# Kernel tuning notes

Measured on AMD Instinct MI355X. Metric: run time of the kernel, lower is better.

## Reference

```python
import jax, jax.numpy as jnp
import numpy as np

NUM_HEADS = 8
EPS = 1e-5


def setup_inputs() -> dict:
    key = jax.random.key(0)
    ks = jax.random.split(key, 12)
    B, S, D = 16384, 12, 512
    s = 1.0 / np.sqrt(D)
    return {
        "x": jax.random.normal(ks[0], (B, S, D), dtype=jnp.float32),
        "Wq": jax.random.uniform(ks[1], (D, D), jnp.float32, -s, s),
        "bq": jax.random.uniform(ks[2], (D,), jnp.float32, -s, s),
        "Wk": jax.random.uniform(ks[3], (D, D), jnp.float32, -s, s),
        "bk": jax.random.uniform(ks[4], (D,), jnp.float32, -s, s),
        "Wv": jax.random.uniform(ks[5], (D, D), jnp.float32, -s, s),
        "bv": jax.random.uniform(ks[6], (D,), jnp.float32, -s, s),
        "adj_bias": jnp.zeros((NUM_HEADS, S, S), dtype=jnp.float32),
        "Wo": jax.random.uniform(ks[7], (D, D), jnp.float32, -s, s),
        "bo": jax.random.uniform(ks[8], (D,), jnp.float32, -s, s),
        "gamma": jnp.ones((D,), dtype=jnp.float32),
        "beta": jnp.zeros((D,), dtype=jnp.float32),
    }


def reference(x, Wq, bq, Wk, bk, Wv, bv, adj_bias, Wo, bo, gamma, beta):
    B, S, D = x.shape
    H = NUM_HEADS
    hd = D // H
    # QKV projections -> (B, H, S, hd)
    def proj(W, b):
        return (jnp.einsum('bsd,de->bse', x, W) + b).reshape(B, S, H, hd).transpose(0, 2, 1, 3)
    q = proj(Wq, bq)
    k = proj(Wk, bk)
    v = proj(Wv, bv)
    # scores with learned adjacency bias: (B, H, S, S)
    scores = jnp.einsum('bhsd,bhtd->bhst', q, k) / np.sqrt(hd).astype(np.float32)
    scores = scores + adj_bias[None, :, :S, :S]
    attn = jax.nn.softmax(scores, axis=-1)  # dropout is identity in eval mode
    out = jnp.einsum('bhst,bhtd->bhsd', attn, v)
    out = out.transpose(0, 2, 1, 3).reshape(B, S, D)
    out = jnp.einsum('bsd,de->bse', out, Wo) + bo
    # residual (in_dim == out_dim) + LayerNorm
    y = out + x
    mu = jnp.mean(y, axis=-1, keepdims=True)
    var = jnp.mean(jnp.square(y - mu), axis=-1, keepdims=True)
    return (y - mu) * jax.lax.rsqrt(var + EPS) * gamma + beta
```

## Files before the change

kernel.cpp:

```cpp
#include <hip/hip_runtime.h>
#include <hip/hip_bf16.h>

#define D_DIM 512
#define S_LEN 12
#define H_NUM 8
#define WMAT 262144

#define G_B1 8
#define ROWS1 96
#define THREADS1 768
#define X_OFF   0
#define Q_OFF   98304
#define K_OFF   110592
#define V_OFF   122880
#define P_OFF   135168
#define SMEM1   142848

#define G_B2 4
#define ROWS2 48
#define THREADS2 512
#define AST_OFF 0
#define RED_OFF 49152
#define MU_OFF  52416
#define SMEM2   52800

typedef __attribute__((ext_vector_type(8))) short bf16x8;
typedef __attribute__((ext_vector_type(4))) float f32x4;

__device__ __forceinline__ unsigned short f2bf(float f) {
    union { float f; unsigned u; } c; c.f = f;
    unsigned r = c.u + 0x7fffu + ((c.u >> 16) & 1u);
    return (unsigned short)(r >> 16);
}
__device__ __forceinline__ float bf2f(unsigned short u) {
    union { unsigned u; float f; } c; c.u = ((unsigned)u) << 16;
    return c.f;
}
__device__ __forceinline__ int xswc(int row, int col) {
    return row * 512 + (((col >> 3) ^ (row & 7)) << 3) + (col & 7);
}
__device__ __forceinline__ int qsw(int row, int col) {
    return row * 64 + (((col >> 3) ^ (row & 7)) << 3) + (col & 7);
}

__global__ void prep_weights(const float* __restrict__ Wq, const float* __restrict__ Wk,
                             const float* __restrict__ Wv, const float* __restrict__ Wo,
                             unsigned short* __restrict__ wt) {
    int idx = blockIdx.x * 256 + threadIdx.x;
    int mat = idx >> 18;
    int rem = idx & (WMAT - 1);
    int e = rem >> 9, d = rem & 511;
    const float* W = (mat == 0) ? Wq : (mat == 1) ? Wk : (mat == 2) ? Wv : Wo;
    wt[idx] = f2bf(W[d * D_DIM + e]);
}

__global__ __launch_bounds__(THREADS1, 3) void qkv_attn(
    const float* __restrict__ x, const unsigned short* __restrict__ wt,
    const float* __restrict__ bq, const float* __restrict__ bk, const float* __restrict__ bv,
    const float* __restrict__ adj, float* __restrict__ aout)
{
    extern __shared__ char smem[];
    unsigned short* Xh = (unsigned short*)(smem + X_OFF);
    unsigned short* Qh = (unsigned short*)(smem + Q_OFF);
    unsigned short* Kh = (unsigned short*)(smem + K_OFF);
    unsigned short* Vh = (unsigned short*)(smem + V_OFF);
    float* Pl = (float*)(smem + P_OFF);

    const int tid  = threadIdx.x;
    const int lane = tid & 63;
    const int w    = tid >> 6;
    const int lr   = lane & 15;
    const int lg   = lane >> 4;
    const int lr12 = (lr < 12) ? lr : 11;
    const size_t row0 = (size_t)blockIdx.x * ROWS1;

    #pragma unroll
    for (int it = 0; it < 16; ++it) {
        int idx = it * THREADS1 + tid;
        int r = idx >> 7, col = (idx & 127) << 2;
        float4 v = *(const float4*)(x + (row0 + r) * (size_t)D_DIM + col);
        ushort4 pk;
        pk.x = f2bf(v.x); pk.y = f2bf(v.y); pk.z = f2bf(v.z); pk.w = f2bf(v.w);
        *(ushort4*)(Xh + xswc(r, col)) = pk;
    }
    __syncthreads();

    const int mat  = w >> 2;
    const int colt = w & 3;
    const int colh = colt * 16 + lr;
    const float* bsel = (mat == 0) ? bq : (mat == 1) ? bk : bv;
    unsigned short* T = (mat == 0) ? Qh : (mat == 1) ? Kh : Vh;
    const int rb = w * S_LEN;

    #pragma unroll 1
    for (int h = 0; h < H_NUM; ++h) {
        f32x4 acc[6];
        #pragma unroll
        for (int mt = 0; mt < 6; ++mt) acc[mt] = (f32x4){0.f, 0.f, 0.f, 0.f};

        const unsigned short* bAp = wt + (size_t)mat * WMAT + (h * 64 + colh) * D_DIM + lg * 8;
        bf16x8 bc = *(const bf16x8*)(bAp);
        #pragma unroll
        for (int ks = 0; ks < 16; ++ks) {
            bf16x8 bn;
            if (ks < 15) bn = *(const bf16x8*)(bAp + (ks + 1) * 32);
            #pragma unroll
            for (int mt = 0; mt < 6; ++mt) {
                bf16x8 af = *(const bf16x8*)(Xh + xswc(mt * 16 + lr, ks * 32 + lg * 8));
                acc[mt] = __builtin_amdgcn_mfma_f32_16x16x32_bf16(af, bc, acc[mt], 0, 0, 0);
            }
            if (ks < 15) bc = bn;
        }
        {
            float bias = bsel[h * 64 + colh];
            #pragma unroll
            for (int mt = 0; mt < 6; ++mt)
                #pragma unroll
                for (int j = 0; j < 4; ++j)
                    T[qsw(mt * 16 + lg * 4 + j, colh)] = f2bf(acc[mt][j] + bias);
        }
        __syncthreads();

        if (w < 8) {
            f32x4 sacc = (f32x4){0.f, 0.f, 0.f, 0.f};
            #pragma unroll
            for (int k2 = 0; k2 < 2; ++k2) {
                bf16x8 ak = *(const bf16x8*)(Kh + qsw(rb + lr12, k2 * 32 + lg * 8));
                bf16x8 aq = *(const bf16x8*)(Qh + qsw(rb + lr12, k2 * 32 + lg * 8));
                sacc = __builtin_amdgcn_mfma_f32_16x16x32_bf16(ak, aq, sacc, 0, 0, 0);
            }
            float ab4[4] = {0.f, 0.f, 0.f, 0.f};
            if (lg < 3 && lr < 12) {
                float4 t4 = *(const float4*)(adj + (h * S_LEN + lr) * S_LEN + lg * 4);
                ab4[0] = t4.x; ab4[1] = t4.y; ab4[2] = t4.z; ab4[3] = t4.w;
            }
            float sc[4], e4[4];
            float m = -1e30f;
            #pragma unroll
            for (int j = 0; j < 4; ++j) {
                int t = lg * 4 + j;
                sc[j] = (t < 12) ? (sacc[j] * 0.125f + ab4[j]) : -1e30f;
                m = fmaxf(m, sc[j]);
            }
            m = fmaxf(m, __shfl_xor(m, 16));
            m = fmaxf(m, __shfl_xor(m, 32));
            float ssum = 0.f;
            #pragma unroll
            for (int j = 0; j < 4; ++j) { e4[j] = __expf(sc[j] - m); ssum += e4[j]; }
            ssum += __shfl_xor(ssum, 16);
            ssum += __shfl_xor(ssum, 32);
            float inv = 1.f / ssum;
            float* Pw = Pl + w * 240;
            if (lr < 12 && lg < 3) {
                f32x4 pvec = (f32x4){e4[0] * inv, e4[1] * inv, e4[2] * inv, e4[3] * inv};
                *(f32x4*)(Pw + lr * 20 + lg * 4) = pvec;
            }
            float vv[12];
            #pragma unroll
            for (int t = 0; t < 12; ++t) vv[t] = bf2f(Vh[qsw(rb + t, lane)]);
            #pragma unroll
            for (int ss = 0; ss < 12; ++ss) {
                f32x4 pa = *(const f32x4*)(Pw + ss * 20);
                f32x4 pb = *(const f32x4*)(Pw + ss * 20 + 4);
                f32x4 pc = *(const f32x4*)(Pw + ss * 20 + 8);
                float o = 0.f;
                #pragma unroll
                for (int t = 0; t < 4; ++t) o += pa[t] * vv[t];
                #pragma unroll
                for (int t = 0; t < 4; ++t) o += pb[t] * vv[4 + t];
                #pragma unroll
                for (int t = 0; t < 4; ++t) o += pc[t] * vv[8 + t];
                aout[(row0 + rb + ss) * (size_t)D_DIM + h * 64 + lane] = o;
            }
        }
        __syncthreads();
    }
}

__global__ __launch_bounds__(THREADS2, 2) void oproj_ln(
    const float* __restrict__ x, const unsigned short* __restrict__ wt,
    const float* __restrict__ bo, const float* __restrict__ gamma,
    const float* __restrict__ beta, float* __restrict__ out)
{
    extern __shared__ char smem[];
    unsigned short* Ast = (unsigned short*)(smem + AST_OFF);
    float* red   = (float*)(smem + RED_OFF);
    float* musig = (float*)(smem + MU_OFF);

    const int tid  = threadIdx.x;
    const int lane = tid & 63;
    const int w    = tid >> 6;
    const int lr   = lane & 15;
    const int lg   = lane >> 4;
    const size_t row0 = (size_t)blockIdx.x * ROWS2;

    #pragma unroll
    for (int it = 0; it < 12; ++it) {
        int idx = it * THREADS2 + tid;
        int r = idx >> 7, col = (idx & 127) << 2;
        float4 v = *(const float4*)(out + (row0 + r) * (size_t)D_DIM + col);
        ushort4 pk;
        pk.x = f2bf(v.x); pk.y = f2bf(v.y); pk.z = f2bf(v.z); pk.w = f2bf(v.w);
        *(ushort4*)(Ast + xswc(r, col)) = pk;
    }
    __syncthreads();

    f32x4 Y[3][4];
    #pragma unroll
    for (int mt = 0; mt < 3; ++mt)
        #pragma unroll
        for (int nt = 0; nt < 4; ++nt) Y[mt][nt] = (f32x4){0.f, 0.f, 0.f, 0.f};

    const unsigned short* obase = wt + (size_t)3 * WMAT + (w * 64 + lr) * D_DIM;
    #pragma unroll 2
    for (int ks = 0; ks < 16; ++ks) {
        bf16x8 afr[3];
        #pragma unroll
        for (int mt = 0; mt < 3; ++mt)
            afr[mt] = *(const bf16x8*)(Ast + xswc(mt * 16 + lr, ks * 32 + lg * 8));
        #pragma unroll
        for (int nt = 0; nt < 4; ++nt) {
            bf16x8 bfr = *(const bf16x8*)(obase + nt * 16 * D_DIM + ks * 32 + lg * 8);
            #pragma unroll
            for (int mt = 0; mt < 3; ++mt)
                Y[mt][nt] = __builtin_amdgcn_mfma_f32_16x16x32_bf16(afr[mt], bfr, Y[mt][nt], 0, 0, 0);
        }
    }

    float bo4[4], gm4[4], bt4[4];
    int cols[4];
    #pragma unroll
    for (int nt = 0; nt < 4; ++nt) {
        cols[nt] = w * 64 + nt * 16 + lr;
        bo4[nt] = bo[cols[nt]]; gm4[nt] = gamma[cols[nt]]; bt4[nt] = beta[cols[nt]];
    }
    #pragma unroll
    for (int mt = 0; mt < 3; ++mt)
        #pragma unroll
        for (int j = 0; j < 4; ++j) {
            int rowl = mt * 16 + lg * 4 + j;
            const float* xrow = x + (row0 + rowl) * (size_t)D_DIM;
            float ps = 0.f, pq = 0.f;
            #pragma unroll
            for (int nt = 0; nt < 4; ++nt) {
                float y = Y[mt][nt][j] + bo4[nt] + xrow[cols[nt]];
                Y[mt][nt][j] = y;
                ps += y; pq += y * y;
            }
            ps += __shfl_xor(ps, 1); pq += __shfl_xor(pq, 1);
            ps += __shfl_xor(ps, 2); pq += __shfl_xor(pq, 2);
            ps += __shfl_xor(ps, 4); pq += __shfl_xor(pq, 4);
            ps += __shfl_xor(ps, 8); pq += __shfl_xor(pq, 8);
            if (lr == 0) { red[rowl * 17 + w * 2] = ps; red[rowl * 17 + w * 2 + 1] = pq; }
        }
    __syncthreads();
    if (tid < ROWS2) {
        float s = 0.f, q = 0.f;
        #pragma unroll
        for (int w8 = 0; w8 < 8; ++w8) { s += red[tid * 17 + w8 * 2]; q += red[tid * 17 + w8 * 2 + 1]; }
        float mu = s * (1.f / 512.f);
        float var = q * (1.f / 512.f) - mu * mu;
        musig[tid * 2] = mu;
        musig[tid * 2 + 1] = rsqrtf(var + 1e-5f);
    }
    __syncthreads();
    #pragma unroll
    for (int mt = 0; mt < 3; ++mt)
        #pragma unroll
        for (int j = 0; j < 4; ++j) {
            int rowl = mt * 16 + lg * 4 + j;
            float mu = musig[rowl * 2], rs = musig[rowl * 2 + 1];
            float* orow = out + (row0 + rowl) * (size_t)D_DIM;
            #pragma unroll
            for (int nt = 0; nt < 4; ++nt)
                orow[cols[nt]] = (Y[mt][nt][j] - mu) * rs * gm4[nt] + bt4[nt];
        }
}

extern "C" void kernel_launch(void* const* d_in, const int* in_sizes, int n_in,
                              void* d_out, int out_size, void* d_ws, size_t ws_size,
                              hipStream_t stream) {
    (void)in_sizes; (void)n_in; (void)out_size; (void)ws_size;
    const float* x     = (const float*)d_in[0];
    const float* Wq    = (const float*)d_in[1];
    const float* bq    = (const float*)d_in[2];
    const float* Wk    = (const float*)d_in[3];
    const float* bk    = (const float*)d_in[4];
    const float* Wv    = (const float*)d_in[5];
    const float* bv    = (const float*)d_in[6];
    const float* adj   = (const float*)d_in[7];
    const float* Wo    = (const float*)d_in[8];
    const float* bo    = (const float*)d_in[9];
    const float* gamma = (const float*)d_in[10];
    const float* beta  = (const float*)d_in[11];
    unsigned short* wt = (unsigned short*)d_ws;
    float* outf = (float*)d_out;

    prep_weights<<<4096, 256, 0, stream>>>(Wq, Wk, Wv, Wo, wt);
    qkv_attn<<<16384 / G_B1, THREADS1, SMEM1, stream>>>(x, wt, bq, bk, bv, adj, outf);
    oproj_ln<<<16384 / G_B2, THREADS2, SMEM2, stream>>>(x, wt, bo, gamma, beta, outf);
}
```

Baseline: 1.095 ms.

## Pad Q/K smem rows, store V transposed, widen oproj block to 96 rows

In the attention kernel, Q and K rows in shared memory are padded to a stride of 72, and V is stored transposed with a stride of 102. This is meant to cut LDS bank conflicts on the score MFMA loads and on the per-lane V reads in the PV loop. The output-projection/LayerNorm kernel now uses 1024-thread blocks over 96 rows, with each wave covering 32 columns and 6 row tiles. That halves weight fragment loads per row, at the cost of more shared memory (about 111 KB) and lower occupancy.

```diff
diff --git a/kernel.cpp b/kernel.cpp
--- a/kernel.cpp
+++ b/kernel.cpp
@@ -9,20 +9,22 @@
 #define G_B1 8
 #define ROWS1 96
 #define THREADS1 768
+#define QS 72
+#define VS 102
 #define X_OFF   0
 #define Q_OFF   98304
-#define K_OFF   110592
-#define V_OFF   122880
-#define P_OFF   135168
-#define SMEM1   142848
-
-#define G_B2 4
-#define ROWS2 48
-#define THREADS2 512
+#define K_OFF   112128
+#define V_OFF   125952
+#define P_OFF   139008
+#define SMEM1   146688
+
+#define G_B2 8
+#define ROWS2 96
+#define THREADS2 1024
 #define AST_OFF 0
-#define RED_OFF 49152
-#define MU_OFF  52416
-#define SMEM2   52800
+#define RED_OFF 98304
+#define MU_OFF  110976
+#define SMEM2   111744
 
 typedef __attribute__((ext_vector_type(8))) short bf16x8;
 typedef __attribute__((ext_vector_type(4))) float f32x4;
@@ -39,8 +41,8 @@
 __device__ __forceinline__ int xswc(int row, int col) {
     return row * 512 + (((col >> 3) ^ (row & 7)) << 3) + (col & 7);
 }
-__device__ __forceinline__ int qsw(int row, int col) {
-    return row * 64 + (((col >> 3) ^ (row & 7)) << 3) + (col & 7);
+__device__ __forceinline__ int qsw72(int row, int col) {
+    return row * QS + (((col >> 3) ^ (row & 7)) << 3) + (col & 7);
 }
 
 __global__ void prep_weights(const float* __restrict__ Wq, const float* __restrict__ Wk,
@@ -63,7 +65,7 @@
     unsigned short* Xh = (unsigned short*)(smem + X_OFF);
     unsigned short* Qh = (unsigned short*)(smem + Q_OFF);
     unsigned short* Kh = (unsigned short*)(smem + K_OFF);
-    unsigned short* Vh = (unsigned short*)(smem + V_OFF);
+    unsigned short* Vt = (unsigned short*)(smem + V_OFF);
     float* Pl = (float*)(smem + P_OFF);
 
     const int tid  = threadIdx.x;
@@ -89,7 +91,6 @@
     const int colt = w & 3;
     const int colh = colt * 16 + lr;
     const float* bsel = (mat == 0) ? bq : (mat == 1) ? bk : bv;
-    unsigned short* T = (mat == 0) ? Qh : (mat == 1) ? Kh : Vh;
     const int rb = w * S_LEN;
 
     #pragma unroll 1
@@ -113,11 +114,24 @@
         }
         {
             float bias = bsel[h * 64 + colh];
-            #pragma unroll
-            for (int mt = 0; mt < 6; ++mt)
-                #pragma unroll
-                for (int j = 0; j < 4; ++j)
-                    T[qsw(mt * 16 + lg * 4 + j, colh)] = f2bf(acc[mt][j] + bias);
+            if (mat == 2) {
+                #pragma unroll
+                for (int mt = 0; mt < 6; ++mt) {
+                    int rbase = mt * 16 + lg * 4;
+                    ushort2 p0, p1;
+                    p0.x = f2bf(acc[mt][0] + bias); p0.y = f2bf(acc[mt][1] + bias);
+                    p1.x = f2bf(acc[mt][2] + bias); p1.y = f2bf(acc[mt][3] + bias);
+                    *(ushort2*)(Vt + colh * VS + rbase)     = p0;
+                    *(ushort2*)(Vt + colh * VS + rbase + 2) = p1;
+                }
+            } else {
+                unsigned short* T = (mat == 0) ? Qh : Kh;
+                #pragma unroll
+                for (int mt = 0; mt < 6; ++mt)
+                    #pragma unroll
+                    for (int j = 0; j < 4; ++j)
+                        T[qsw72(mt * 16 + lg * 4 + j, colh)] = f2bf(acc[mt][j] + bias);
+            }
         }
         __syncthreads();
 
@@ -125,8 +139,8 @@
             f32x4 sacc = (f32x4){0.f, 0.f, 0.f, 0.f};
             #pragma unroll
             for (int k2 = 0; k2 < 2; ++k2) {
-                bf16x8 ak = *(const bf16x8*)(Kh + qsw(rb + lr12, k2 * 32 + lg * 8));
-                bf16x8 aq = *(const bf16x8*)(Qh + qsw(rb + lr12, k2 * 32 + lg * 8));
+                bf16x8 ak = *(const bf16x8*)(Kh + qsw72(rb + lr12, k2 * 32 + lg * 8));
+                bf16x8 aq = *(const bf16x8*)(Qh + qsw72(rb + lr12, k2 * 32 + lg * 8));
                 sacc = __builtin_amdgcn_mfma_f32_16x16x32_bf16(ak, aq, sacc, 0, 0, 0);
             }
             float ab4[4] = {0.f, 0.f, 0.f, 0.f};
@@ -157,7 +171,7 @@
             }
             float vv[12];
             #pragma unroll
-            for (int t = 0; t < 12; ++t) vv[t] = bf2f(Vh[qsw(rb + t, lane)]);
+            for (int t = 0; t < 12; ++t) vv[t] = bf2f(Vt[lane * VS + rb + t]);
             #pragma unroll
             for (int ss = 0; ss < 12; ++ss) {
                 f32x4 pa = *(const f32x4*)(Pw + ss * 20);
@@ -177,7 +191,7 @@
     }
 }
 
-__global__ __launch_bounds__(THREADS2, 2) void oproj_ln(
+__global__ __launch_bounds__(THREADS2) void oproj_ln(
     const float* __restrict__ x, const unsigned short* __restrict__ wt,
     const float* __restrict__ bo, const float* __restrict__ gamma,
     const float* __restrict__ beta, float* __restrict__ out)
@@ -205,45 +219,45 @@
     }
     __syncthreads();
 
-    f32x4 Y[3][4];
-    #pragma unroll
-    for (int mt = 0; mt < 3; ++mt)
-        #pragma unroll
-        for (int nt = 0; nt < 4; ++nt) Y[mt][nt] = (f32x4){0.f, 0.f, 0.f, 0.f};
-
-    const unsigned short* obase = wt + (size_t)3 * WMAT + (w * 64 + lr) * D_DIM;
+    f32x4 Y[6][2];
+    #pragma unroll
+    for (int mt = 0; mt < 6; ++mt)
+        #pragma unroll
+        for (int nt = 0; nt < 2; ++nt) Y[mt][nt] = (f32x4){0.f, 0.f, 0.f, 0.f};
+
+    const unsigned short* obase = wt + (size_t)3 * WMAT + (w * 32 + lr) * D_DIM;
     #pragma unroll 2
     for (int ks = 0; ks < 16; ++ks) {
-        bf16x8 afr[3];
-        #pragma unroll
-        for (int mt = 0; mt < 3; ++mt)
+        bf16x8 afr[6];
+        #pragma unroll
+        for (int mt = 0; mt < 6; ++mt)
             afr[mt] = *(const bf16x8*)(Ast + xswc(mt * 16 + lr, ks * 32 + lg * 8));
         #pragma unroll
-        for (int nt = 0; nt < 4; ++nt) {
+        for (int nt = 0; nt < 2; ++nt) {
             bf16x8 bfr = *(const bf16x8*)(obase + nt * 16 * D_DIM + ks * 32 + lg * 8);
             #pragma unroll
-            for (int mt = 0; mt < 3; ++mt)
+            for (int mt = 0; mt < 6; ++mt)
                 Y[mt][nt] = __builtin_amdgcn_mfma_f32_16x16x32_bf16(afr[mt], bfr, Y[mt][nt], 0, 0, 0);
         }
     }
 
-    float bo4[4], gm4[4], bt4[4];
-    int cols[4];
-    #pragma unroll
-    for (int nt = 0; nt < 4; ++nt) {
-        cols[nt] = w * 64 + nt * 16 + lr;
-        bo4[nt] = bo[cols[nt]]; gm4[nt] = gamma[cols[nt]]; bt4[nt] = beta[cols[nt]];
-    }
-    #pragma unroll
-    for (int mt = 0; mt < 3; ++mt)
+    float bo2[2], gm2[2], bt2[2];
+    int cols[2];
+    #pragma unroll
+    for (int nt = 0; nt < 2; ++nt) {
+        cols[nt] = w * 32 + nt * 16 + lr;
+        bo2[nt] = bo[cols[nt]]; gm2[nt] = gamma[cols[nt]]; bt2[nt] = beta[cols[nt]];
+    }
+    #pragma unroll
+    for (int mt = 0; mt < 6; ++mt)
         #pragma unroll
         for (int j = 0; j < 4; ++j) {
             int rowl = mt * 16 + lg * 4 + j;
             const float* xrow = x + (row0 + rowl) * (size_t)D_DIM;
             float ps = 0.f, pq = 0.f;
             #pragma unroll
-            for (int nt = 0; nt < 4; ++nt) {
-                float y = Y[mt][nt][j] + bo4[nt] + xrow[cols[nt]];
+            for (int nt = 0; nt < 2; ++nt) {
+                float y = Y[mt][nt][j] + bo2[nt] + xrow[cols[nt]];
                 Y[mt][nt][j] = y;
                 ps += y; pq += y * y;
             }
@@ -251,13 +265,13 @@
             ps += __shfl_xor(ps, 2); pq += __shfl_xor(pq, 2);
             ps += __shfl_xor(ps, 4); pq += __shfl_xor(pq, 4);
             ps += __shfl_xor(ps, 8); pq += __shfl_xor(pq, 8);
-            if (lr == 0) { red[rowl * 17 + w * 2] = ps; red[rowl * 17 + w * 2 + 1] = pq; }
+            if (lr == 0) { red[rowl * 33 + w * 2] = ps; red[rowl * 33 + w * 2 + 1] = pq; }
         }
     __syncthreads();
     if (tid < ROWS2) {
         float s = 0.f, q = 0.f;
         #pragma unroll
-        for (int w8 = 0; w8 < 8; ++w8) { s += red[tid * 17 + w8 * 2]; q += red[tid * 17 + w8 * 2 + 1]; }
+        for (int w16 = 0; w16 < 16; ++w16) { s += red[tid * 33 + w16 * 2]; q += red[tid * 33 + w16 * 2 + 1]; }
         float mu = s * (1.f / 512.f);
         float var = q * (1.f / 512.f) - mu * mu;
         musig[tid * 2] = mu;
@@ -265,15 +279,15 @@
     }
     __syncthreads();
     #pragma unroll
-    for (int mt = 0; mt < 3; ++mt)
+    for (int mt = 0; mt < 6; ++mt)
         #pragma unroll
         for (int j = 0; j < 4; ++j) {
             int rowl = mt * 16 + lg * 4 + j;
             float mu = musig[rowl * 2], rs = musig[rowl * 2 + 1];
             float* orow = out + (row0 + rowl) * (size_t)D_DIM;
             #pragma unroll
-            for (int nt = 0; nt < 4; ++nt)
-                orow[cols[nt]] = (Y[mt][nt][j] - mu) * rs * gm4[nt] + bt4[nt];
+            for (int nt = 0; nt < 2; ++nt)
+                orow[cols[nt]] = (Y[mt][nt][j] - mu) * rs * gm2[nt] + bt2[nt];
         }
 }
 
```

Result: no change. 1.113 ms (+1.7%).

## Retile QKV-attention kernel to 48 rows with 4 heads per pass

Applied to the files above, without the earlier changes.

The first kernel now handles 48 rows per block instead of 96. Each wave computes a full 64-column head tile (3x4 MFMA tiles) for one of four heads per pass, so each weight fragment is reused across 3 row tiles instead of 6. Heads are processed two groups at a time instead of one at a time, which cuts the number of block barriers. Attention work is spread over all 12 waves via a strided loop over 16 (head, batch-group) tasks. Shared memory per block drops slightly, but the number of blocks doubles, so total weight traffic from global/L2 per row may rise.

```diff
diff --git a/kernel.cpp b/kernel.cpp
--- a/kernel.cpp
+++ b/kernel.cpp
@@ -6,15 +6,14 @@
 #define H_NUM 8
 #define WMAT 262144
 
-#define G_B1 8
-#define ROWS1 96
+#define G_B1 4
+#define ROWS1 48
 #define THREADS1 768
 #define X_OFF   0
-#define Q_OFF   98304
-#define K_OFF   110592
-#define V_OFF   122880
-#define P_OFF   135168
-#define SMEM1   142848
+#define QKV_OFF 49152
+#define TBLK    3072
+#define P_OFF   122880
+#define SMEM1   138240
 
 #define G_B2 4
 #define ROWS2 48
@@ -39,7 +38,7 @@
 __device__ __forceinline__ int xswc(int row, int col) {
     return row * 512 + (((col >> 3) ^ (row & 7)) << 3) + (col & 7);
 }
-__device__ __forceinline__ int qsw(int row, int col) {
+__device__ __forceinline__ int qsw64(int row, int col) {
     return row * 64 + (((col >> 3) ^ (row & 7)) << 3) + (col & 7);
 }
 
@@ -60,10 +59,8 @@
     const float* __restrict__ adj, float* __restrict__ aout)
 {
     extern __shared__ char smem[];
-    unsigned short* Xh = (unsigned short*)(smem + X_OFF);
-    unsigned short* Qh = (unsigned short*)(smem + Q_OFF);
-    unsigned short* Kh = (unsigned short*)(smem + K_OFF);
-    unsigned short* Vh = (unsigned short*)(smem + V_OFF);
+    unsigned short* Xh  = (unsigned short*)(smem + X_OFF);
+    unsigned short* QKV = (unsigned short*)(smem + QKV_OFF);
     float* Pl = (float*)(smem + P_OFF);
 
     const int tid  = threadIdx.x;
@@ -75,7 +72,7 @@
     const size_t row0 = (size_t)blockIdx.x * ROWS1;
 
     #pragma unroll
-    for (int it = 0; it < 16; ++it) {
+    for (int it = 0; it < 8; ++it) {
         int idx = it * THREADS1 + tid;
         int r = idx >> 7, col = (idx & 127) << 2;
         float4 v = *(const float4*)(x + (row0 + r) * (size_t)D_DIM + col);
@@ -85,48 +82,74 @@
     }
     __syncthreads();
 
-    const int mat  = w >> 2;
-    const int colt = w & 3;
-    const int colh = colt * 16 + lr;
+    const int mat = w >> 2;
+    const int hh  = w & 3;
     const float* bsel = (mat == 0) ? bq : (mat == 1) ? bk : bv;
-    unsigned short* T = (mat == 0) ? Qh : (mat == 1) ? Kh : Vh;
-    const int rb = w * S_LEN;
+    unsigned short* Tw = QKV + (mat * 4 + hh) * TBLK;
 
     #pragma unroll 1
-    for (int h = 0; h < H_NUM; ++h) {
-        f32x4 acc[6];
-        #pragma unroll
-        for (int mt = 0; mt < 6; ++mt) acc[mt] = (f32x4){0.f, 0.f, 0.f, 0.f};
-
-        const unsigned short* bAp = wt + (size_t)mat * WMAT + (h * 64 + colh) * D_DIM + lg * 8;
-        bf16x8 bc = *(const bf16x8*)(bAp);
+    for (int hg = 0; hg < 2; ++hg) {
+        const int hglob = hg * 4 + hh;
+        f32x4 acc[3][4];
+        #pragma unroll
+        for (int mt = 0; mt < 3; ++mt)
+            #pragma unroll
+            for (int nt = 0; nt < 4; ++nt) acc[mt][nt] = (f32x4){0.f, 0.f, 0.f, 0.f};
+
+        const unsigned short* bp[4];
+        bf16x8 bc[4];
+        #pragma unroll
+        for (int nt = 0; nt < 4; ++nt) {
+            bp[nt] = wt + (size_t)mat * WMAT + (hglob * 64 + nt * 16 + lr) * D_DIM + lg * 8;
+            bc[nt] = *(const bf16x8*)bp[nt];
+        }
         #pragma unroll
         for (int ks = 0; ks < 16; ++ks) {
-            bf16x8 bn;
-            if (ks < 15) bn = *(const bf16x8*)(bAp + (ks + 1) * 32);
-            #pragma unroll
-            for (int mt = 0; mt < 6; ++mt) {
-                bf16x8 af = *(const bf16x8*)(Xh + xswc(mt * 16 + lr, ks * 32 + lg * 8));
-                acc[mt] = __builtin_amdgcn_mfma_f32_16x16x32_bf16(af, bc, acc[mt], 0, 0, 0);
-            }
-            if (ks < 15) bc = bn;
-        }
-        {
-            float bias = bsel[h * 64 + colh];
-            #pragma unroll
-            for (int mt = 0; mt < 6; ++mt)
+            bf16x8 bn[4];
+            if (ks < 15) {
+                #pragma unroll
+                for (int nt = 0; nt < 4; ++nt)
+                    bn[nt] = *(const bf16x8*)(bp[nt] + (ks + 1) * 32);
+            }
+            bf16x8 af[3];
+            #pragma unroll
+            for (int mt = 0; mt < 3; ++mt)
+                af[mt] = *(const bf16x8*)(Xh + xswc(mt * 16 + lr, ks * 32 + lg * 8));
+            #pragma unroll
+            for (int nt = 0; nt < 4; ++nt)
+                #pragma unroll
+                for (int mt = 0; mt < 3; ++mt)
+                    acc[mt][nt] = __builtin_amdgcn_mfma_f32_16x16x32_bf16(af[mt], bc[nt], acc[mt][nt], 0, 0, 0);
+            if (ks < 15) {
+                #pragma unroll
+                for (int nt = 0; nt < 4; ++nt) bc[nt] = bn[nt];
+            }
+        }
+        #pragma unroll
+        for (int nt = 0; nt < 4; ++nt) {
+            float bias = bsel[hglob * 64 + nt * 16 + lr];
+            #pragma unroll
+            for (int mt = 0; mt < 3; ++mt)
                 #pragma unroll
                 for (int j = 0; j < 4; ++j)
-                    T[qsw(mt * 16 + lg * 4 + j, colh)] = f2bf(acc[mt][j] + bias);
+                    Tw[qsw64(mt * 16 + lg * 4 + j, nt * 16 + lr)] = f2bf(acc[mt][nt][j] + bias);
         }
         __syncthreads();
 
-        if (w < 8) {
+        for (int t = w; t < 16; t += 12) {
+            const int ab = t & 3;
+            const int th = t >> 2;
+            const int h  = hg * 4 + th;
+            const int rbA = ab * S_LEN;
+            const unsigned short* Qb = QKV + (0 * 4 + th) * TBLK;
+            const unsigned short* Kb = QKV + (1 * 4 + th) * TBLK;
+            const unsigned short* Vb = QKV + (2 * 4 + th) * TBLK;
+
             f32x4 sacc = (f32x4){0.f, 0.f, 0.f, 0.f};
             #pragma unroll
             for (int k2 = 0; k2 < 2; ++k2) {
-                bf16x8 ak = *(const bf16x8*)(Kh + qsw(rb + lr12, k2 * 32 + lg * 8));
-                bf16x8 aq = *(const bf16x8*)(Qh + qsw(rb + lr12, k2 * 32 + lg * 8));
+                bf16x8 ak = *(const bf16x8*)(Kb + qsw64(rbA + lr12, k2 * 32 + lg * 8));
+                bf16x8 aq = *(const bf16x8*)(Qb + qsw64(rbA + lr12, k2 * 32 + lg * 8));
                 sacc = __builtin_amdgcn_mfma_f32_16x16x32_bf16(ak, aq, sacc, 0, 0, 0);
             }
             float ab4[4] = {0.f, 0.f, 0.f, 0.f};
@@ -138,8 +161,8 @@
             float m = -1e30f;
             #pragma unroll
             for (int j = 0; j < 4; ++j) {
-                int t = lg * 4 + j;
-                sc[j] = (t < 12) ? (sacc[j] * 0.125f + ab4[j]) : -1e30f;
+                int tt = lg * 4 + j;
+                sc[j] = (tt < 12) ? (sacc[j] * 0.125f + ab4[j]) : -1e30f;
                 m = fmaxf(m, sc[j]);
             }
             m = fmaxf(m, __shfl_xor(m, 16));
@@ -150,14 +173,14 @@
             ssum += __shfl_xor(ssum, 16);
             ssum += __shfl_xor(ssum, 32);
             float inv = 1.f / ssum;
-            float* Pw = Pl + w * 240;
+            float* Pw = Pl + t * 240;
             if (lr < 12 && lg < 3) {
                 f32x4 pvec = (f32x4){e4[0] * inv, e4[1] * inv, e4[2] * inv, e4[3] * inv};
                 *(f32x4*)(Pw + lr * 20 + lg * 4) = pvec;
             }
             float vv[12];
             #pragma unroll
-            for (int t = 0; t < 12; ++t) vv[t] = bf2f(Vh[qsw(rb + t, lane)]);
+            for (int t2 = 0; t2 < 12; ++t2) vv[t2] = bf2f(Vb[qsw64(rbA + t2, lane)]);
             #pragma unroll
             for (int ss = 0; ss < 12; ++ss) {
                 f32x4 pa = *(const f32x4*)(Pw + ss * 20);
@@ -165,15 +188,15 @@
                 f32x4 pc = *(const f32x4*)(Pw + ss * 20 + 8);
                 float o = 0.f;
                 #pragma unroll
-                for (int t = 0; t < 4; ++t) o += pa[t] * vv[t];
-                #pragma unroll
-                for (int t = 0; t < 4; ++t) o += pb[t] * vv[4 + t];
-                #pragma unroll
-                for (int t = 0; t < 4; ++t) o += pc[t] * vv[8 + t];
-                aout[(row0 + rb + ss) * (size_t)D_DIM + h * 64 + lane] = o;
-            }
-        }
-        __syncthreads();
+                for (int t2 = 0; t2 < 4; ++t2) o += pa[t2] * vv[t2];
+                #pragma unroll
+                for (int t2 = 0; t2 < 4; ++t2) o += pb[t2] * vv[4 + t2];
+                #pragma unroll
+                for (int t2 = 0; t2 < 4; ++t2) o += pc[t2] * vv[8 + t2];
+                aout[(row0 + rbA + ss) * (size_t)D_DIM + h * 64 + lane] = o;
+            }
+        }
+        if (hg == 0) __syncthreads();
     }
 }
 
```

After: 1.758 ms. 1.61x slower.
